# Kernel tuning notes

Hardware: AMD Instinct MI355X
Metric: run time of the kernel (lower is better)

Reference implementation:

```python
import jax, jax.numpy as jnp
import numpy as np

RATIO = 0.8

def _sage(x, src, dst, mask, Wl, bl, Wr, n):
    # PyG SAGEConv (mean aggr): lin_l(mean_j x_j) + lin_r(x_i); bias on lin_l only
    msg = x[src] * mask[:, None]                               # [E, d]
    agg = jax.ops.segment_sum(msg, dst, num_segments=n)       # [n, d]
    cnt = jax.ops.segment_sum(mask, dst, num_segments=n)      # [n]
    mean = agg / jnp.maximum(cnt, 1.0)[:, None]
    return mean @ Wl + bl + x @ Wr

def _topk(x, src, dst, mask, w, Bg, Npg):
    # PyG TopKPooling: score = tanh(x.w/||w||); keep top ceil(ratio*N) per graph; x' = x[perm]*score
    K = int(np.ceil(RATIO * Npg))
    score = jnp.tanh((x @ w) / jnp.linalg.norm(w))             # [Bg*Npg]
    vals, idx = jax.lax.top_k(score.reshape(Bg, Npg), K)       # [Bg, K]
    perm = (idx + (jnp.arange(Bg) * Npg)[:, None]).reshape(-1)
    x_new = x[perm] * vals.reshape(-1, 1)                      # [Bg*K, d]
    new_id = jnp.full((Bg * Npg,), -1, jnp.int32).at[perm].set(jnp.arange(Bg * K, dtype=jnp.int32))
    s2 = new_id[src]; d2 = new_id[dst]
    valid = mask * ((s2 >= 0) & (d2 >= 0)).astype(x.dtype)     # filter_adj as a mask
    return x_new, jnp.maximum(s2, 0), jnp.maximum(d2, 0), valid, K

def _readout(x, Bg, K):
    # global_max_pool || global_mean_pool (equal-sized graphs -> reshape)
    xr = x.reshape(Bg, K, x.shape[-1])
    return jnp.concatenate([xr.max(axis=1), xr.mean(axis=1)], axis=-1)

def _forward(x, edge_index, params, Bg, Npg):
    (Wl1, bl1, Wr1, pw1, Wl2, bl2, Wr2, pw2, Wl3, bl3, Wr3, pw3,
     W1, b1, W2, b2, W3, b3) = params
    src = edge_index[0]; dst = edge_index[1]
    mask = jnp.ones(src.shape, x.dtype)
    n = Bg * Npg
    h = jax.nn.relu(_sage(x, src, dst, mask, Wl1, bl1, Wr1, n))
    h, src, dst, mask, K = _topk(h, src, dst, mask, pw1, Bg, Npg)
    x1 = _readout(h, Bg, K)
    h = jax.nn.relu(_sage(h, src, dst, mask, Wl2, bl2, Wr2, Bg * K))
    h, src, dst, mask, K = _topk(h, src, dst, mask, pw2, Bg, K)
    x2 = _readout(h, Bg, K)
    h = jax.nn.relu(_sage(h, src, dst, mask, Wl3, bl3, Wr3, Bg * K))
    h, src, dst, mask, K = _topk(h, src, dst, mask, pw3, Bg, K)
    x3 = _readout(h, Bg, K)
    s = x1 + x2 + x3                                           # [Bg, 256]
    s = jax.nn.relu(s @ W1 + b1)
    s = jax.nn.relu(s @ W2 + b2)                               # dropout: eval mode no-op
    return jax.nn.sigmoid(s @ W3 + b3).squeeze(-1)             # [Bg]

def setup_inputs() -> dict:
    key = jax.random.key(0)
    ks = jax.random.split(key, 24)
    B, N, DEG, D = 64, 1024, 16, 128
    x = jax.random.normal(ks[0], (B * N, D), jnp.float32)
    off = (jnp.arange(B) * N)[:, None]
    src = (jax.random.randint(ks[1], (B, N * DEG), 0, N) + off).reshape(-1)
    dst = (jax.random.randint(ks[2], (B, N * DEG), 0, N) + off).reshape(-1)
    edge_index = jnp.stack([src, dst]).astype(jnp.int32)
    s = 1.0 / np.sqrt(D)
    def w(k, shp, sc): return jax.random.normal(k, shp, jnp.float32) * sc
    inp = dict(x=x, edge_index=edge_index)
    for i, k0 in zip((1, 2, 3), (3, 7, 11)):
        inp[f'Wl{i}'] = w(ks[k0], (D, D), s)
        inp[f'bl{i}'] = jnp.zeros((D,), jnp.float32)
        inp[f'Wr{i}'] = w(ks[k0 + 1], (D, D), s)
        inp[f'pw{i}'] = w(ks[k0 + 2], (D,), s)
    inp['W1'] = w(ks[15], (256, 128), 1.0 / np.sqrt(256)); inp['b1'] = jnp.zeros((128,), jnp.float32)
    inp['W2'] = w(ks[16], (128, 64), 1.0 / np.sqrt(128)); inp['b2'] = jnp.zeros((64,), jnp.float32)
    inp['W3'] = w(ks[17], (64, 1), 1.0 / np.sqrt(64)); inp['b3'] = jnp.zeros((1,), jnp.float32)
    inp['B'] = B; inp['N'] = N
    return inp

def reference(x, edge_index, Wl1, bl1, Wr1, pw1, Wl2, bl2, Wr2, pw2, Wl3, bl3, Wr3, pw3, W1, b1, W2, b2, W3, b3, B, N):
    params = (Wl1, bl1, Wr1, pw1, Wl2, bl2, Wr2, pw2, Wl3, bl3, Wr3, pw3, W1, b1, W2, b2, W3, b3)
    return _forward(x, edge_index, params, B, N)
```

## Files before the change

kernel.cpp:

```cpp
#include <hip/hip_runtime.h>
#include <math.h>

#define D       128
#define NGRAPH  64
#define N0      1024
#define NE      (1<<20)
#define EPG     (NE/NGRAPH)
#define NTOT    (NGRAPH*N0)
#define ASLOT   64

__device__ float g_h[NTOT*D];
__device__ float g_h2[NTOT*D];
__device__ unsigned short g_mh[NTOT*D];
__device__ unsigned short g_ml[NTOT*D];
__device__ unsigned short g_xh[NTOT*D];
__device__ unsigned short g_xl[NTOT*D];
__device__ unsigned short g_wbh[3*128*256];
__device__ unsigned short g_wbl[3*128*256];
__device__ int   g_adjA[NTOT*ASLOT];
__device__ int   g_adjB[NTOT*ASLOT];
__device__ int   g_cntA[NTOT];
__device__ int   g_cntB[NTOT];
__device__ float g_dot[NTOT];
__device__ float g_pwnorm[3];
__device__ int   g_selidx[NGRAPH*820];
__device__ float g_selval[NGRAPH*820];
__device__ int   g_newid[NTOT];
__device__ float g_pool[3*NGRAPH*8*256];
typedef __attribute__((ext_vector_type(8))) short bf16x8;
typedef __attribute__((ext_vector_type(8))) unsigned short ushort8;
typedef __attribute__((ext_vector_type(4))) float f32x4;

__device__ inline unsigned short f2bf_rne(float f) {
    unsigned u = __float_as_uint(f);
    u += 0x7FFF + ((u >> 16) & 1);
    return (unsigned short)(u >> 16);
}
__device__ inline void split2(float v, unsigned short& h, unsigned short& l) {
    h = f2bf_rne(v);
    l = f2bf_rne(v - __uint_as_float((unsigned)h << 16));
}

__global__ void k_prep_w(const float* __restrict__ Wl1, const float* __restrict__ Wr1,
                         const float* __restrict__ Wl2, const float* __restrict__ Wr2,
                         const float* __restrict__ Wl3, const float* __restrict__ Wr3) {
    int t = blockIdx.x * 256 + threadIdx.x;
    int r = t >> 15, rem = t & 32767;
    int c = rem >> 8, k = rem & 255;
    const float* WlR = (r == 0) ? Wl1 : (r == 1) ? Wl2 : Wl3;
    const float* WrR = (r == 0) ? Wr1 : (r == 1) ? Wr2 : Wr3;
    float v = (k < 128) ? WlR[k * 128 + c] : WrR[(k - 128) * 128 + c];
    split2(v, g_wbh[t], g_wbl[t]);
}

__global__ void k_norms(const float* __restrict__ p1, const float* __restrict__ p2,
                        const float* __restrict__ p3) {
    int r = blockIdx.x, lane = threadIdx.x;
    const float* p = (r == 0) ? p1 : (r == 1) ? p2 : p3;
    float a = p[lane], b = p[lane + 64];
    float s = a * a + b * b;
    for (int off = 32; off; off >>= 1) s += __shfl_xor(s, off);
    if (lane == 0) g_pwnorm[r] = sqrtf(s);
}

__global__ void k_prep_x(const float* __restrict__ x) {
    int t = blockIdx.x * 256 + threadIdx.x;
    float4 v = ((const float4*)x)[t];
    ushort4 h4, l4;
    split2(v.x, h4.x, l4.x); split2(v.y, h4.y, l4.y);
    split2(v.z, h4.z, l4.z); split2(v.w, h4.w, l4.w);
    ((ushort4*)g_xh)[t] = h4;
    ((ushort4*)g_xl)[t] = l4;
}

__global__ __launch_bounds__(1024) void k_badj0(const int* __restrict__ ei) {
    __shared__ int s_fill[N0];
    int g = blockIdx.x, tid = threadIdx.x;
    s_fill[tid] = 0;
    __syncthreads();
    int e0 = g * EPG;
#pragma unroll
    for (int i = 0; i < EPG / 1024; i++) {
        int e = e0 + i * 1024 + tid;
        int s = ei[e];
        int d = ei[NE + e];
        int slot = atomicAdd(&s_fill[d - g * N0], 1);
        if (slot < ASLOT) g_adjA[(size_t)d * ASLOT + slot] = s;
    }
    __syncthreads();
    g_cntA[g * N0 + tid] = min(s_fill[tid], ASLOT);
}

__global__ __launch_bounds__(256) void k_compact(int n_new, int dir) {
    int wid = threadIdx.x >> 6, lane = threadIdx.x & 63;
    int nj = blockIdx.x * 4 + wid;
    if (nj >= n_new) return;
    int old = g_selidx[nj];
    const int* adjO = dir ? g_adjB : g_adjA;
    const int* cntO = dir ? g_cntB : g_cntA;
    int* adjN = dir ? g_adjA : g_adjB;
    int* cntN = dir ? g_cntA : g_cntB;
    int cnt = cntO[old];
    int m = -1;
    if (lane < cnt) m = g_newid[adjO[(size_t)old * ASLOT + lane]];
    unsigned long long mask = __ballot(m >= 0);
    int pos = __popcll(mask & ((1ull << lane) - 1ull));
    if (m >= 0) adjN[(size_t)nj * ASLOT + pos] = m;
    if (lane == 0) cntN[nj] = __popcll(mask);
}

__global__ __launch_bounds__(256) void k_aggregate(const float* __restrict__ x_in,
                                                   int use_input, int ab, int M, int BPG) {
    const float* X = use_input ? x_in : g_h;
    const int* adj = ab ? g_adjB : g_adjA;
    const int* cntp = ab ? g_cntB : g_cntA;
    int b = blockIdx.x;
    int j = b >> 3;
    int g = (b & 7) + 8 * (j / BPG);
    int ib = j % BPG;
    int wid = threadIdx.x >> 6, lane = threadIdx.x & 63;
    int half = lane >> 5, li = lane & 31;
    int local = ib * 8 + wid * 2 + half;
    int node = g * M + local;
    int cnt = (local < M) ? cntp[node] : 0;
    int cnt2 = max(cnt, __shfl_xor(cnt, 32));
    float ax = 0.f, ay = 0.f, az = 0.f, aw = 0.f;
    const float4* Xp = (const float4*)X;
    size_t abase = (size_t)node * ASLOT;
    for (int base = 0; base < cnt2; base += 32) {
        int a = (base + li < cnt) ? adj[abase + base + li] : -1;
        int mm = min(cnt2 - base, 32);
        int mmr = (mm + 3) & ~3;
        for (int i = 0; i < mmr; i += 4) {
            int s0 = __shfl(a, half * 32 + i + 0);
            int s1 = __shfl(a, half * 32 + i + 1);
            int s2 = __shfl(a, half * 32 + i + 2);
            int s3 = __shfl(a, half * 32 + i + 3);
            float4 v0 = Xp[(size_t)max(s0, 0) * 32 + li];
            float4 v1 = Xp[(size_t)max(s1, 0) * 32 + li];
            float4 v2 = Xp[(size_t)max(s2, 0) * 32 + li];
            float4 v3 = Xp[(size_t)max(s3, 0) * 32 + li];
            float m0 = (s0 >= 0) ? 1.f : 0.f, m1 = (s1 >= 0) ? 1.f : 0.f;
            float m2 = (s2 >= 0) ? 1.f : 0.f, m3 = (s3 >= 0) ? 1.f : 0.f;
            ax += m0 * v0.x + m1 * v1.x + m2 * v2.x + m3 * v3.x;
            ay += m0 * v0.y + m1 * v1.y + m2 * v2.y + m3 * v3.y;
            az += m0 * v0.z + m1 * v1.z + m2 * v2.z + m3 * v3.z;
            aw += m0 * v0.w + m1 * v1.w + m2 * v2.w + m3 * v3.w;
        }
    }
    if (local < M) {
        float inv = 1.f / (float)max(cnt, 1);
        ushort4 h4, l4;
        split2(ax * inv, h4.x, l4.x); split2(ay * inv, h4.y, l4.y);
        split2(az * inv, h4.z, l4.z); split2(aw * inv, h4.w, l4.w);
        *(ushort4*)&g_mh[(size_t)node * 128 + li * 4] = h4;
        *(ushort4*)&g_ml[(size_t)node * 128 + li * 4] = l4;
        if (li == 0) g_dot[node] = 0.f;
    }
}

__global__ __launch_bounds__(256, 2) void k_gemm(int r,
                                                 const float* __restrict__ bl,
                                                 const float* __restrict__ pw) {
    __shared__ __align__(16) unsigned short sa_hi[128 * 40];
    __shared__ __align__(16) unsigned short sa_lo[128 * 40];
    __shared__ __align__(16) unsigned short sb_hi[128 * 40];
    __shared__ __align__(16) unsigned short sb_lo[128 * 40];
    const unsigned short* Wbh = g_wbh + r * 32768;
    const unsigned short* Wbl = g_wbl + r * 32768;
    int tid = threadIdx.x;
    int row0 = blockIdx.x * 128;
    int wid = tid >> 6, lane = tid & 63;
    int wr = wid >> 1, wc = wid & 1;
    int lrow = lane & 15, kgrp = lane >> 4;

    f32x4 acc[4][4];
#pragma unroll
    for (int mi = 0; mi < 4; mi++)
#pragma unroll
        for (int ni = 0; ni < 4; ni++)
#pragma unroll
            for (int q = 0; q < 4; q++) acc[mi][ni][q] = 0.f;

    for (int kc = 0; kc < 256; kc += 32) {
        const unsigned short* Ah = (kc < 128) ? g_mh : g_xh;
        const unsigned short* Al = (kc < 128) ? g_ml : g_xl;
        int kloc = kc & 127;
        __syncthreads();
#pragma unroll
        for (int i = 0; i < 2; i++) {
            int f = tid + i * 256;
            int row = f >> 2, kq = f & 3;
            size_t src = (size_t)(row0 + row) * 128 + kloc + kq * 8;
            *(ushort8*)&sa_hi[row * 40 + kq * 8] = *(const ushort8*)&Ah[src];
            *(ushort8*)&sa_lo[row * 40 + kq * 8] = *(const ushort8*)&Al[src];
        }
#pragma unroll
        for (int i = 0; i < 2; i++) {
            int f = tid + i * 256;
            int c = f >> 2, kq = f & 3;
            size_t src = (size_t)c * 256 + kc + kq * 8;
            *(ushort8*)&sb_hi[c * 40 + kq * 8] = *(const ushort8*)&Wbh[src];
            *(ushort8*)&sb_lo[c * 40 + kq * 8] = *(const ushort8*)&Wbl[src];
        }
        __syncthreads();
        bf16x8 ah[4], al[4], bh[4], blo[4];
#pragma unroll
        for (int mi = 0; mi < 4; mi++) {
            int rr = wr * 64 + mi * 16 + lrow;
            ah[mi] = *(const bf16x8*)&sa_hi[rr * 40 + kgrp * 8];
            al[mi] = *(const bf16x8*)&sa_lo[rr * 40 + kgrp * 8];
        }
#pragma unroll
        for (int ni = 0; ni < 4; ni++) {
            int c = wc * 64 + ni * 16 + lrow;
            bh[ni]  = *(const bf16x8*)&sb_hi[c * 40 + kgrp * 8];
            blo[ni] = *(const bf16x8*)&sb_lo[c * 40 + kgrp * 8];
        }
#pragma unroll
        for (int mi = 0; mi < 4; mi++)
#pragma unroll
            for (int ni = 0; ni < 4; ni++) {
                acc[mi][ni] = __builtin_amdgcn_mfma_f32_16x16x32_bf16(ah[mi], bh[ni],  acc[mi][ni], 0, 0, 0);
                acc[mi][ni] = __builtin_amdgcn_mfma_f32_16x16x32_bf16(ah[mi], blo[ni], acc[mi][ni], 0, 0, 0);
                acc[mi][ni] = __builtin_amdgcn_mfma_f32_16x16x32_bf16(al[mi], bh[ni],  acc[mi][ni], 0, 0, 0);
            }
    }
    float pwv[4];
#pragma unroll
    for (int ni = 0; ni < 4; ni++) pwv[ni] = pw[wc * 64 + ni * 16 + lrow];
#pragma unroll
    for (int mi = 0; mi < 4; mi++) {
        float dotq[4] = {0.f, 0.f, 0.f, 0.f};
#pragma unroll
        for (int ni = 0; ni < 4; ni++) {
            int c = wc * 64 + ni * 16 + lrow;
            float b = bl[c];
#pragma unroll
            for (int q = 0; q < 4; q++) {
                float v = fmaxf(acc[mi][ni][q] + b, 0.f);
                g_h2[(size_t)(row0 + wr * 64 + mi * 16 + kgrp * 4 + q) * 128 + c] = v;
                dotq[q] += v * pwv[ni];
            }
        }
#pragma unroll
        for (int q = 0; q < 4; q++) {
            float dv = dotq[q];
            dv += __shfl_xor(dv, 1); dv += __shfl_xor(dv, 2);
            dv += __shfl_xor(dv, 4); dv += __shfl_xor(dv, 8);
            if (lrow == 0)
                atomicAdd(&g_dot[row0 + wr * 64 + mi * 16 + kgrp * 4 + q], dv);
        }
    }
}

__global__ void k_topk(int M, int K, int rr) {
    __shared__ float sc[1024];
    __shared__ int   id[1024];
    int g = blockIdx.x, tid = threadIdx.x;
    float invn = 1.f / g_pwnorm[rr];
    for (int i = tid; i < 1024; i += 512) {
        sc[i] = (i < M) ? g_dot[g * M + i] : -INFINITY;
        id[i] = i;
    }
    for (int i = tid; i < M; i += 512) g_newid[g * M + i] = -1;
    __syncthreads();
    for (int k = 2; k <= 1024; k <<= 1) {
        for (int j = k >> 1; j > 0; j >>= 1) {
            for (int i = tid; i < 1024; i += 512) {
                int ixj = i ^ j;
                if (ixj > i) {
                    bool desc = ((i & k) == 0);
                    float a = sc[i], b = sc[ixj];
                    bool sw = desc ? (a < b) : (a > b);
                    if (sw) {
                        sc[i] = b; sc[ixj] = a;
                        int t = id[i]; id[i] = id[ixj]; id[ixj] = t;
                    }
                }
            }
            __syncthreads();
        }
    }
    for (int j = tid; j < K; j += 512) {
        int li = id[j];
        g_selidx[g * K + j] = g * M + li;
        g_selval[g * K + j] = tanhf(sc[j] * invn);
        g_newid[g * M + li] = g * K + j;
    }
}

__global__ void k_gather_pool(int K, int rr) {
    int g = blockIdx.x, chunk = blockIdx.y;
    int cs = (K + 7) / 8;
    int j0 = chunk * cs, j1 = min(K, j0 + cs);
    int tid = threadIdx.x;
    int c = tid & 127, half = tid >> 7;
    float mx = -INFINITY, sm = 0.f;
    for (int j = j0 + half; j < j1; j += 2) {
        int srcRow = g_selidx[g * K + j];
        float v = g_h2[(size_t)srcRow * 128 + c] * g_selval[g * K + j];
        size_t o = (size_t)(g * K + j) * 128 + c;
        g_h[o] = v;
        split2(v, g_xh[o], g_xl[o]);
        mx = fmaxf(mx, v); sm += v;
    }
    __shared__ float smx[256], ssm[256];
    smx[tid] = mx; ssm[tid] = sm;
    __syncthreads();
    if (half == 0) {
        mx = fmaxf(mx, smx[tid + 128]);
        sm += ssm[tid + 128];
        g_pool[((rr * NGRAPH + g) * 8 + chunk) * 256 + c] = mx;
        g_pool[((rr * NGRAPH + g) * 8 + chunk) * 256 + 128 + c] = sm;
    }
}

__global__ void k_mlp(const float* __restrict__ W1, const float* __restrict__ b1,
                      const float* __restrict__ W2, const float* __restrict__ b2,
                      const float* __restrict__ W3, const float* __restrict__ b3,
                      float* __restrict__ out, int K0, int K1, int K2) {
    int g = blockIdx.x, tid = threadIdx.x;
    __shared__ float s_sh[256], h1[128], h2v[64], red[128];
    float Kf[3] = {(float)K0, (float)K1, (float)K2};
    float accmax = 0.f, accmean = 0.f;
    for (int r = 0; r < 3; r++) {
        float mx = -INFINITY, sm = 0.f;
        for (int ch = 0; ch < 8; ch++) {
            const float* p = &g_pool[((r * NGRAPH + g) * 8 + ch) * 256];
            mx = fmaxf(mx, p[tid]);
            sm += p[128 + tid];
        }
        accmax += mx;
        accmean += sm / Kf[r];
    }
    s_sh[tid] = accmax; s_sh[128 + tid] = accmean;
    __syncthreads();
    float a = 0.f;
    for (int k = 0; k < 256; k++) a += s_sh[k] * W1[k * 128 + tid];
    h1[tid] = fmaxf(a + b1[tid], 0.f);
    __syncthreads();
    if (tid < 64) {
        float a2 = 0.f;
        for (int k = 0; k < 128; k++) a2 += h1[k] * W2[k * 64 + tid];
        h2v[tid] = fmaxf(a2 + b2[tid], 0.f);
    }
    __syncthreads();
    red[tid] = (tid < 64) ? h2v[tid] * W3[tid] : 0.f;
    __syncthreads();
    for (int s = 64; s > 0; s >>= 1) {
        if (tid < s) red[tid] += red[tid + s];
        __syncthreads();
    }
    if (tid == 0) {
        float z = red[0] + b3[0];
        out[g] = 1.f / (1.f + expf(-z));
    }
}

extern "C" void kernel_launch(void* const* d_in, const int* in_sizes, int n_in,
                              void* d_out, int out_size, void* d_ws, size_t ws_size,
                              hipStream_t stream) {
    const float* x  = (const float*)d_in[0];
    const int*   ei = (const int*)d_in[1];
    const float* Wl[3] = {(const float*)d_in[2], (const float*)d_in[6],  (const float*)d_in[10]};
    const float* bl[3] = {(const float*)d_in[3], (const float*)d_in[7],  (const float*)d_in[11]};
    const float* Wr[3] = {(const float*)d_in[4], (const float*)d_in[8],  (const float*)d_in[12]};
    const float* pw[3] = {(const float*)d_in[5], (const float*)d_in[9],  (const float*)d_in[13]};
    const float* W1 = (const float*)d_in[14]; const float* b1 = (const float*)d_in[15];
    const float* W2 = (const float*)d_in[16]; const float* b2 = (const float*)d_in[17];
    const float* W3 = (const float*)d_in[18]; const float* b3 = (const float*)d_in[19];
    float* out = (float*)d_out;

    const int Ms[3] = {1024, 820, 656};
    const int Ks[3] = {820, 656, 525};

    k_prep_w<<<384, 256, 0, stream>>>(Wl[0], Wr[0], Wl[1], Wr[1], Wl[2], Wr[2]);
    k_norms<<<3, 64, 0, stream>>>(pw[0], pw[1], pw[2]);
    k_prep_x<<<NTOT * D / 4 / 256, 256, 0, stream>>>(x);

    for (int r = 0; r < 3; r++) {
        int M = Ms[r], K = Ks[r];
        int n = NGRAPH * M;
        int BPG = (M + 7) / 8;
        int ab = (r == 1) ? 1 : 0;
        if (r == 0)
            k_badj0<<<NGRAPH, 1024, 0, stream>>>(ei);
        else
            k_compact<<<(n + 3) / 4, 256, 0, stream>>>(n, r - 1);
        k_aggregate<<<NGRAPH * BPG, 256, 0, stream>>>(x, (r == 0) ? 1 : 0, ab, M, BPG);
        k_gemm<<<n / 128, 256, 0, stream>>>(r, bl[r], pw[r]);
        k_topk<<<NGRAPH, 512, 0, stream>>>(M, K, r);
        k_gather_pool<<<dim3(NGRAPH, 8), 256, 0, stream>>>(K, r);
    }
    k_mlp<<<NGRAPH, 128, 0, stream>>>(W1, b1, W2, b2, W3, b3, out,
                                      Ks[0], Ks[1], Ks[2]);
}
```

Baseline: 510.3 us.

## Stage per-graph feature chunks in LDS for neighbor mean aggregation

The aggregation kernel now has each block load one graph's 32-column slice of node features into shared memory (padded rows), then gathers neighbor rows from LDS instead of global memory. Edges are graph-local, so every neighbor index falls inside the tile. Each half-wave handles one node, with 4 sub-groups splitting the neighbors and combining partial sums by shuffle reduction. This replaces random global float4 gathers with LDS reads, but the grid shrinks to 256 blocks of 512 threads at one block per CU, each using about 132KB of LDS, which limits occupancy and latency hiding.

```diff
diff --git a/kernel.cpp b/kernel.cpp
--- a/kernel.cpp
+++ b/kernel.cpp
@@ -109,53 +109,60 @@
     if (lane == 0) cntN[nj] = __popcll(mask);
 }
 
-__global__ __launch_bounds__(256) void k_aggregate(const float* __restrict__ x_in,
-                                                   int use_input, int ab, int M, int BPG) {
+__global__ __launch_bounds__(512, 1) void k_aggregate(const float* __restrict__ x_in,
+                                                      int use_input, int ab, int M) {
+    __shared__ float tile[N0 * 33];
     const float* X = use_input ? x_in : g_h;
     const int* adj = ab ? g_adjB : g_adjA;
     const int* cntp = ab ? g_cntB : g_cntA;
     int b = blockIdx.x;
-    int j = b >> 3;
-    int g = (b & 7) + 8 * (j / BPG);
-    int ib = j % BPG;
-    int wid = threadIdx.x >> 6, lane = threadIdx.x & 63;
+    int g = (b & 7) + 8 * (b >> 5);
+    int chunk = (b >> 3) & 3;
+    int c0 = chunk * 32;
+    int gbase = g * M;
+    int tid = threadIdx.x;
+    for (int f = tid; f < M * 8; f += 512) {
+        int row = f >> 3, cq = f & 7;
+        *(float4*)&tile[row * 33 + cq * 4] =
+            *(const float4*)&X[(size_t)(gbase + row) * 128 + c0 + cq * 4];
+    }
+    __syncthreads();
+    int lane = tid & 63, wid = tid >> 6;
     int half = lane >> 5, li = lane & 31;
-    int local = ib * 8 + wid * 2 + half;
-    int node = g * M + local;
-    int cnt = (local < M) ? cntp[node] : 0;
-    int cnt2 = max(cnt, __shfl_xor(cnt, 32));
-    float ax = 0.f, ay = 0.f, az = 0.f, aw = 0.f;
-    const float4* Xp = (const float4*)X;
-    size_t abase = (size_t)node * ASLOT;
-    for (int base = 0; base < cnt2; base += 32) {
-        int a = (base + li < cnt) ? adj[abase + base + li] : -1;
-        int mm = min(cnt2 - base, 32);
-        int mmr = (mm + 3) & ~3;
-        for (int i = 0; i < mmr; i += 4) {
-            int s0 = __shfl(a, half * 32 + i + 0);
-            int s1 = __shfl(a, half * 32 + i + 1);
-            int s2 = __shfl(a, half * 32 + i + 2);
-            int s3 = __shfl(a, half * 32 + i + 3);
-            float4 v0 = Xp[(size_t)max(s0, 0) * 32 + li];
-            float4 v1 = Xp[(size_t)max(s1, 0) * 32 + li];
-            float4 v2 = Xp[(size_t)max(s2, 0) * 32 + li];
-            float4 v3 = Xp[(size_t)max(s3, 0) * 32 + li];
-            float m0 = (s0 >= 0) ? 1.f : 0.f, m1 = (s1 >= 0) ? 1.f : 0.f;
-            float m2 = (s2 >= 0) ? 1.f : 0.f, m3 = (s3 >= 0) ? 1.f : 0.f;
-            ax += m0 * v0.x + m1 * v1.x + m2 * v2.x + m3 * v3.x;
-            ay += m0 * v0.y + m1 * v1.y + m2 * v2.y + m3 * v3.y;
-            az += m0 * v0.z + m1 * v1.z + m2 * v2.z + m3 * v3.z;
-            aw += m0 * v0.w + m1 * v1.w + m2 * v2.w + m3 * v3.w;
-        }
-    }
-    if (local < M) {
-        float inv = 1.f / (float)max(cnt, 1);
-        ushort4 h4, l4;
-        split2(ax * inv, h4.x, l4.x); split2(ay * inv, h4.y, l4.y);
-        split2(az * inv, h4.z, l4.z); split2(aw * inv, h4.w, l4.w);
-        *(ushort4*)&g_mh[(size_t)node * 128 + li * 4] = h4;
-        *(ushort4*)&g_ml[(size_t)node * 128 + li * 4] = l4;
-        if (li == 0) g_dot[node] = 0.f;
+    int sg = li >> 3, cl = li & 7;
+    for (int local = wid * 2 + half; local < M; local += 16) {
+        int node = gbase + local;
+        int cnt = cntp[node];
+        size_t abase = (size_t)node * ASLOT;
+        int a0 = adj[abase + li];
+        int a1 = adj[abase + 32 + li];
+        float ax = 0.f, ay = 0.f, az = 0.f, aw = 0.f;
+        for (int i16 = 0; i16 < cnt; i16 += 16) {
+            int areg = (i16 < 32) ? a0 : a1;
+#pragma unroll
+            for (int q = 0; q < 4; q++) {
+                int idx = i16 + q * 4 + sg;
+                int s = __shfl(areg, half * 32 + (idx & 31));
+                bool ok = (idx < cnt);
+                int sl = (ok ? s : node) - gbase;
+                float4 v = *(const float4*)&tile[sl * 33 + cl * 4];
+                float m = ok ? 1.f : 0.f;
+                ax += m * v.x; ay += m * v.y; az += m * v.z; aw += m * v.w;
+            }
+        }
+        ax += __shfl_xor(ax, 8);  ay += __shfl_xor(ay, 8);
+        az += __shfl_xor(az, 8);  aw += __shfl_xor(aw, 8);
+        ax += __shfl_xor(ax, 16); ay += __shfl_xor(ay, 16);
+        az += __shfl_xor(az, 16); aw += __shfl_xor(aw, 16);
+        if (sg == 0) {
+            float inv = 1.f / (float)max(cnt, 1);
+            ushort4 h4, l4;
+            split2(ax * inv, h4.x, l4.x); split2(ay * inv, h4.y, l4.y);
+            split2(az * inv, h4.z, l4.z); split2(aw * inv, h4.w, l4.w);
+            *(ushort4*)&g_mh[(size_t)node * 128 + c0 + cl * 4] = h4;
+            *(ushort4*)&g_ml[(size_t)node * 128 + c0 + cl * 4] = l4;
+            if (chunk == 0 && cl == 0) g_dot[node] = 0.f;
+        }
     }
 }
 
@@ -382,13 +389,12 @@
     for (int r = 0; r < 3; r++) {
         int M = Ms[r], K = Ks[r];
         int n = NGRAPH * M;
-        int BPG = (M + 7) / 8;
         int ab = (r == 1) ? 1 : 0;
         if (r == 0)
             k_badj0<<<NGRAPH, 1024, 0, stream>>>(ei);
         else
             k_compact<<<(n + 3) / 4, 256, 0, stream>>>(n, r - 1);
-        k_aggregate<<<NGRAPH * BPG, 256, 0, stream>>>(x, (r == 0) ? 1 : 0, ab, M, BPG);
+        k_aggregate<<<NGRAPH * 4, 512, 0, stream>>>(x, (r == 0) ? 1 : 0, ab, M);
         k_gemm<<<n / 128, 256, 0, stream>>>(r, bl[r], pw[r]);
         k_topk<<<NGRAPH, 512, 0, stream>>>(M, K, r);
         k_gather_pool<<<dim3(NGRAPH, 8), 256, 0, stream>>>(K, r);
```

Measured after the change: 642.3 us. 25.9% more time.
